# Optimization experiments

Hardware: AMD Instinct MI355X
Metric: run time of the kernel (lower is better)

The kernel has to match this reference:

```python
import jax, jax.numpy as jnp
import numpy as np
from jax import lax

MARGIN = 0.3
BIGF = 1e9


def _pairwise_dist(x):
    # dist[i,j] = ||x_i - x_j||, clamped at 1e-12 before sqrt (as in torch code)
    sq = jnp.sum(x * x, axis=1)
    d = sq[:, None] + sq[None, :] - 2.0 * (x @ x.T)
    return jnp.sqrt(jnp.clip(d, 1e-12))


def _hard_mining(dist, targets):
    is_pos = targets[:, None] == targets[None, :]
    ap = jnp.where(is_pos, dist, jnp.asarray(-BIGF, dist.dtype))
    an = jnp.where(is_pos, jnp.asarray(BIGF, dist.dtype), dist)
    dist_ap = jnp.max(ap, axis=1)
    p_inds = jnp.argmax(ap, axis=1)
    dist_an = jnp.min(an, axis=1)
    n_inds = jnp.argmin(an, axis=1)
    return dist_ap, dist_an, p_inds, n_inds


def _batch_euclidean(x, y):
    # x: [N,m,d], y: [N,n,d] -> [N,m,n]
    xx = jnp.sum(x * x, axis=-1)[:, :, None]
    yy = jnp.sum(y * y, axis=-1)[:, None, :]
    d = xx + yy - 2.0 * jnp.einsum('nmd,nkd->nmk', x, y)
    return jnp.sqrt(jnp.clip(d, 1e-12))


def _shortest_dist(dmat):
    # DTW-style shortest path over [m,n] grid, batched over N: dp[i,j] = d[i,j] + min(dp[i-1,j], dp[i,j-1])
    N, m, n = dmat.shape
    big = jnp.asarray(BIGF, dmat.dtype)
    init_row = jnp.full((N, n), big, dmat.dtype).at[:, 0].set(0.0)  # virtual row -1: only (0,0) reachable

    def row_step(prev_row, drow):  # prev_row,drow: [N,n]
        def col_step(left, un):  # left: [N]
            up, d = un
            cur = d + jnp.minimum(up, left)
            return cur, cur
        _, cols = lax.scan(col_step, jnp.full((N,), big, dmat.dtype), (prev_row.T, drow.T))
        return cols.T, None

    last_row, _ = lax.scan(row_step, init_row, jnp.moveaxis(dmat, 1, 0))
    return last_row[:, -1]


def _batch_local_dist(x, y):
    d = _batch_euclidean(x, y)
    d = jnp.tanh(d * 0.5)  # == (exp(d)-1)/(exp(d)+1), numerically safe
    return _shortest_dist(d)


def _margin_ranking(dist_an, dist_ap, margin):
    # MarginRankingLoss with y=1: mean(relu(margin - (dist_an - dist_ap)))
    return jnp.mean(jnp.maximum(0.0, margin + dist_ap - dist_an))


def setup_inputs() -> dict:
    key = jax.random.key(0)
    k1, k2 = jax.random.split(key)
    N, D = 512, 2048
    LD, PARTS = 128, 8
    K = 4  # instances per identity (PK sampling)
    inputs = jax.random.normal(k1, (N, D), dtype=jnp.float32)
    local_features = jax.random.normal(k2, (N, LD, PARTS), dtype=jnp.float32)
    targets = jnp.arange(N, dtype=jnp.int64) // K
    return {"inputs": inputs, "targets": targets, "local_features": local_features}


def reference(inputs, targets, local_features):
    dist = _pairwise_dist(inputs)
    dist_ap, dist_an, p_inds, n_inds = _hard_mining(dist, targets)
    global_loss = _margin_ranking(dist_an, dist_ap, MARGIN)
    lf = jnp.transpose(local_features, (0, 2, 1))  # [N, parts, local_dim]
    local_ap = _batch_local_dist(lf, lf[p_inds])
    local_an = _batch_local_dist(lf, lf[n_inds])
    local_loss = _margin_ranking(local_an, local_ap, MARGIN)
    return (global_loss, local_loss)
```

## Files before the change

### kernel.cpp

```cpp
#include <hip/hip_runtime.h>
#include <math.h>

#define MARGIN 0.3f
#define BIGF 1e9f
#define NN 512
#define DD 2048
#define LDIM 128
#define PARTS 8

typedef __attribute__((ext_vector_type(8))) __bf16 bf16x8;
typedef __attribute__((ext_vector_type(4))) float f32x4;

__device__ __forceinline__ void cvt8(const float4 a, const float4 b,
                                     bf16x8& h, bf16x8& l) {
    float f[8] = {a.x, a.y, a.z, a.w, b.x, b.y, b.z, b.w};
#pragma unroll
    for (int e = 0; e < 8; e++) {
        __bf16 hh = (__bf16)f[e];
        h[e] = hh;
        l[e] = (__bf16)(f[e] - (float)hh);
    }
}

__global__ __launch_bounds__(256, 2) void k_gram(
    const float* __restrict__ X, float* __restrict__ Gp,
    float* __restrict__ ndiag, float* gsum, float* lsum, unsigned* counter)
{
    __shared__ __bf16 Ah[4096], Al[4096], Bh[4096], Bl[4096];

    int bid = blockIdx.x;
    int tj = bid & 7, ti = (bid >> 3) & 7, ks = bid >> 6;
    int t = threadIdx.x;
    int w = t >> 6, lane = t & 63;
    int wr = w >> 1, wc = w & 1;

    if (bid == 0 && t == 0) { *gsum = 0.0f; *lsum = 0.0f; *counter = 0u; }

    int m = t >> 7;
    int r = (t >> 1) & 63;
    int kst = t & 1;
    int grow = (m ? tj : ti) * 64 + r;
    const float4* gp4 = (const float4*)(X + (size_t)grow * DD + ks * 256 + kst * 32);
    int ebase = kst * 2048 + (r >> 4) * 512 + (r & 15) * 8;
    __bf16* hb = (m ? Bh : Ah) + ebase;
    __bf16* lb = (m ? Bl : Al) + ebase;

    float4 cur[8];
#pragma unroll
    for (int q = 0; q < 8; q++) cur[q] = gp4[q];

    f32x4 acc00 = {0.f, 0.f, 0.f, 0.f};
    f32x4 acc01 = {0.f, 0.f, 0.f, 0.f};
    f32x4 acc10 = {0.f, 0.f, 0.f, 0.f};
    f32x4 acc11 = {0.f, 0.f, 0.f, 0.f};

#pragma unroll
    for (int it = 0; it < 4; ++it) {
        if (it > 0) __syncthreads();
#pragma unroll
        for (int jg = 0; jg < 4; jg++) {
            bf16x8 h, l;
            cvt8(cur[2 * jg], cur[2 * jg + 1], h, l);
            *(bf16x8*)(hb + jg * 128) = h;
            *(bf16x8*)(lb + jg * 128) = l;
        }
        if (it < 3) {
            const float4* np = gp4 + (it + 1) * 16;
#pragma unroll
            for (int q = 0; q < 8; q++) cur[q] = np[q];
        }
        __syncthreads();

#pragma unroll
        for (int kstep = 0; kstep < 2; kstep++) {
            const bf16x8* fAh = (const bf16x8*)&Ah[kstep * 2048 + wr * 1024];
            const bf16x8* fAl = (const bf16x8*)&Al[kstep * 2048 + wr * 1024];
            const bf16x8* fBh = (const bf16x8*)&Bh[kstep * 2048 + wc * 1024];
            const bf16x8* fBl = (const bf16x8*)&Bl[kstep * 2048 + wc * 1024];
            bf16x8 ah0 = fAh[lane], ah1 = fAh[lane + 64];
            bf16x8 al0 = fAl[lane], al1 = fAl[lane + 64];
            bf16x8 bh0 = fBh[lane], bh1 = fBh[lane + 64];
            bf16x8 bl0 = fBl[lane], bl1 = fBl[lane + 64];

            acc00 = __builtin_amdgcn_mfma_f32_16x16x32_bf16(ah0, bh0, acc00, 0, 0, 0);
            acc00 = __builtin_amdgcn_mfma_f32_16x16x32_bf16(ah0, bl0, acc00, 0, 0, 0);
            acc00 = __builtin_amdgcn_mfma_f32_16x16x32_bf16(al0, bh0, acc00, 0, 0, 0);

            acc01 = __builtin_amdgcn_mfma_f32_16x16x32_bf16(ah0, bh1, acc01, 0, 0, 0);
            acc01 = __builtin_amdgcn_mfma_f32_16x16x32_bf16(ah0, bl1, acc01, 0, 0, 0);
            acc01 = __builtin_amdgcn_mfma_f32_16x16x32_bf16(al0, bh1, acc01, 0, 0, 0);

            acc10 = __builtin_amdgcn_mfma_f32_16x16x32_bf16(ah1, bh0, acc10, 0, 0, 0);
            acc10 = __builtin_amdgcn_mfma_f32_16x16x32_bf16(ah1, bl0, acc10, 0, 0, 0);
            acc10 = __builtin_amdgcn_mfma_f32_16x16x32_bf16(al1, bh0, acc10, 0, 0, 0);

            acc11 = __builtin_amdgcn_mfma_f32_16x16x32_bf16(ah1, bh1, acc11, 0, 0, 0);
            acc11 = __builtin_amdgcn_mfma_f32_16x16x32_bf16(ah1, bl1, acc11, 0, 0, 0);
            acc11 = __builtin_amdgcn_mfma_f32_16x16x32_bf16(al1, bh1, acc11, 0, 0, 0);
        }
    }

    int rbase = ti * 64 + wr * 32 + ((lane >> 4) << 2);
    int cbase = tj * 64 + wc * 32 + (lane & 15);
    float* gb = Gp + (size_t)ks * NN * NN;
    f32x4 accs[2][2] = {{acc00, acc01}, {acc10, acc11}};
#pragma unroll
    for (int g = 0; g < 2; g++)
#pragma unroll
        for (int h = 0; h < 2; h++)
#pragma unroll
            for (int rr = 0; rr < 4; rr++)
                gb[(size_t)(rbase + g * 16 + rr) * NN + cbase + h * 16] = accs[g][h][rr];

    if (ti == tj && wr == wc && ((lane >> 4) == ((lane & 15) >> 2))) {
        int rr = lane & 3;
        int row0 = rbase + rr;
        ndiag[ks * NN + row0]      = acc00[rr];
        ndiag[ks * NN + row0 + 16] = acc11[rr];
    }
}

__global__ __launch_bounds__(256) void k_mine_local(
    const float* __restrict__ Gp, const float* __restrict__ ndiag,
    const int* __restrict__ tg, const float* __restrict__ LF,
    float* gsum, float* lsum, unsigned* counter, float* __restrict__ out)
{
    __shared__ float sdiag[NN];
    __shared__ float s_apv[4]; __shared__ int s_api[4];
    __shared__ float s_anv[4]; __shared__ int s_ani[4];
    __shared__ int sh_pn[2];
    __shared__ float A[LDIM * PARTS];
    __shared__ float B[2][LDIM * PARTS];
    __shared__ float dtm[2][64];
    __shared__ float res[2];

    int i = blockIdx.x;
    int t = threadIdx.x;

    float d0 = 0.f, d1 = 0.f;
#pragma unroll
    for (int ks = 0; ks < 8; ks++) {
        d0 += ndiag[ks * NN + t];
        d1 += ndiag[ks * NN + t + 256];
    }
    sdiag[t] = d0;
    sdiag[t + 256] = d1;
    __syncthreads();

    float ni = sdiag[i];
    int tgt_i = tg[i];

    float apv = -BIGF; int api = 0x7fffffff;
    float anv =  BIGF; int ani = 0x7fffffff;

#pragma unroll
    for (int jj = 0; jj < 2; jj++) {
        int j = t + jj * 256;
        float g = 0.f;
#pragma unroll
        for (int ks = 0; ks < 8; ks++)
            g += Gp[(size_t)ks * NN * NN + (size_t)i * NN + j];
        float nj = (jj == 0) ? d0 : d1;
        float dd = ni + nj - 2.0f * g;
        float dist = sqrtf(fmaxf(dd, 1e-12f));
        bool pos = (tg[j] == tgt_i);
        float a = pos ? dist : -BIGF;
        if (a > apv || (a == apv && j < api)) { apv = a; api = j; }
        float b = pos ? BIGF : dist;
        if (b < anv || (b == anv && j < ani)) { anv = b; ani = j; }
    }
    for (int off = 32; off > 0; off >>= 1) {
        float av = __shfl_down(apv, off); int ai = __shfl_down(api, off);
        if (av > apv || (av == apv && ai < api)) { apv = av; api = ai; }
        float nv = __shfl_down(anv, off); int nid = __shfl_down(ani, off);
        if (nv < anv || (nv == anv && nid < ani)) { anv = nv; ani = nid; }
    }
    int lane = t & 63, wid = t >> 6;
    if (lane == 0) { s_apv[wid] = apv; s_api[wid] = api;
                     s_anv[wid] = anv; s_ani[wid] = ani; }
    __syncthreads();
    if (t == 0) {
        apv = s_apv[0]; api = s_api[0]; anv = s_anv[0]; ani = s_ani[0];
        for (int wv = 1; wv < 4; wv++) {
            float av = s_apv[wv]; int ai = s_api[wv];
            if (av > apv || (av == apv && ai < api)) { apv = av; api = ai; }
            float nv = s_anv[wv]; int nid = s_ani[wv];
            if (nv < anv || (nv == anv && nid < ani)) { anv = nv; ani = nid; }
        }
        sh_pn[0] = api;
        sh_pn[1] = ani;
        atomicAdd(gsum, fmaxf(0.0f, MARGIN + apv - anv));
    }
    __syncthreads();

    int w = t >> 6;
    ((float4*)A)[t] = ((const float4*)(LF + (size_t)i * LDIM * PARTS))[t];
    if (w < 2) {
        int ind = sh_pn[w];
        const float4* B4 = (const float4*)(LF + (size_t)ind * LDIM * PARTS);
        float4* Bw = (float4*)B[w];
        Bw[lane]       = B4[lane];
        Bw[lane + 64]  = B4[lane + 64];
        Bw[lane + 128] = B4[lane + 128];
        Bw[lane + 192] = B4[lane + 192];
    }
    __syncthreads();

    if (w < 2) {
        int p = lane >> 3, q = lane & 7;
        float acc = 0.0f;
        const float* Bw = B[w];
        for (int d = 0; d < LDIM; d++) {
            float diff = A[d * PARTS + p] - Bw[d * PARTS + q];
            acc = fmaf(diff, diff, acc);
        }
        float dist = sqrtf(fmaxf(acc, 1e-12f));
        dtm[w][p * 8 + q] = tanhf(0.5f * dist);
    }
    __syncthreads();

    if ((t == 0) || (t == 64)) {
        const float* dm = dtm[w];
        float dp[8];
        dp[0] = dm[0];
        for (int j = 1; j < 8; j++) dp[j] = dp[j - 1] + dm[j];
        for (int rr = 1; rr < 8; rr++) {
            dp[0] += dm[rr * 8];
            for (int j = 1; j < 8; j++)
                dp[j] = dm[rr * 8 + j] + fminf(dp[j], dp[j - 1]);
        }
        res[w] = dp[7];
    }
    __syncthreads();

    if (t == 0) {
        float l = fmaxf(0.0f, MARGIN + res[0] - res[1]);
        atomicAdd(lsum, l);
        __threadfence();
        unsigned old = atomicAdd(counter, 1u);
        if (old == (NN - 1)) {
            __threadfence();
            float ls = atomicAdd(lsum, 0.0f);
            float gs = atomicAdd(gsum, 0.0f);
            out[0] = gs * (1.0f / NN);
            out[1] = ls * (1.0f / NN);
        }
    }
}

extern "C" void kernel_launch(void* const* d_in, const int* in_sizes, int n_in,
                              void* d_out, int out_size, void* d_ws, size_t ws_size,
                              hipStream_t stream)
{
    const float* X  = (const float*)d_in[0];
    const int*   tg = (const int*)d_in[1];
    const float* LF = (const float*)d_in[2];
    float* out = (float*)d_out;

    char* ws = (char*)d_ws;
    float*    Gp      = (float*)ws;
    float*    ndiag   = (float*)(ws + (8u << 20));
    float*    gsum    = (float*)(ws + (8u << 20) + 16384);
    float*    lsum    = (float*)(ws + (8u << 20) + 16388);
    unsigned* counter = (unsigned*)(ws + (8u << 20) + 16392);

    k_gram<<<512, 256, 0, stream>>>(X, Gp, ndiag, gsum, lsum, counter);
    k_mine_local<<<512, 256, 0, stream>>>(Gp, ndiag, tg, LF, gsum, lsum, counter, out);
}
```

Measured before the change: 96.93 us.

## Fuse gram and mining kernels with a software grid barrier

Merges the split-K gram kernel and the hard-mining/local-distance kernel into one launch, separated by a global atomic spin barrier over all 512 blocks. Counters are now zeroed with a memset on the stream instead of inside the kernel. This removes the second kernel launch and the gap between launches, but it adds a memset, a grid-wide spin wait, and more shared memory per block. The barrier depends on all 512 blocks being resident at once, which the 2-blocks-per-SM launch bound is meant to allow.

Result: slower. 195.4 us (+101.6%).

```diff
diff --git a/kernel.cpp b/kernel.cpp
--- a/kernel.cpp
+++ b/kernel.cpp
@@ -22,19 +22,27 @@
     }
 }
 
-__global__ __launch_bounds__(256, 2) void k_gram(
-    const float* __restrict__ X, float* __restrict__ Gp,
-    float* __restrict__ ndiag, float* gsum, float* lsum, unsigned* counter)
+__global__ __launch_bounds__(256, 2) void k_fused(
+    const float* __restrict__ X, const int* __restrict__ tg,
+    const float* __restrict__ LF, float* __restrict__ Gp,
+    float* __restrict__ ndiag, float* gsum, float* lsum,
+    unsigned* ticket, unsigned* bar, float* __restrict__ out)
 {
     __shared__ __bf16 Ah[4096], Al[4096], Bh[4096], Bl[4096];
+    __shared__ float sdiag[NN];
+    __shared__ float s_apv[4]; __shared__ int s_api[4];
+    __shared__ float s_anv[4]; __shared__ int s_ani[4];
+    __shared__ int sh_pn[2];
+    __shared__ float A2[LDIM * PARTS];
+    __shared__ float B2[2][LDIM * PARTS];
+    __shared__ float dtm[2][64];
+    __shared__ float res[2];
 
     int bid = blockIdx.x;
     int tj = bid & 7, ti = (bid >> 3) & 7, ks = bid >> 6;
     int t = threadIdx.x;
     int w = t >> 6, lane = t & 63;
     int wr = w >> 1, wc = w & 1;
-
-    if (bid == 0 && t == 0) { *gsum = 0.0f; *lsum = 0.0f; *counter = 0u; }
 
     int m = t >> 7;
     int r = (t >> 1) & 63;
@@ -118,30 +126,25 @@
         ndiag[ks * NN + row0]      = acc00[rr];
         ndiag[ks * NN + row0 + 16] = acc11[rr];
     }
-}
-
-__global__ __launch_bounds__(256) void k_mine_local(
-    const float* __restrict__ Gp, const float* __restrict__ ndiag,
-    const int* __restrict__ tg, const float* __restrict__ LF,
-    float* gsum, float* lsum, unsigned* counter, float* __restrict__ out)
-{
-    __shared__ float sdiag[NN];
-    __shared__ float s_apv[4]; __shared__ int s_api[4];
-    __shared__ float s_anv[4]; __shared__ int s_ani[4];
-    __shared__ int sh_pn[2];
-    __shared__ float A[LDIM * PARTS];
-    __shared__ float B[2][LDIM * PARTS];
-    __shared__ float dtm[2][64];
-    __shared__ float res[2];
-
-    int i = blockIdx.x;
-    int t = threadIdx.x;
+
+    __syncthreads();
+    if (t == 0) {
+        __threadfence();
+        __hip_atomic_fetch_add(bar, 1u, __ATOMIC_RELEASE, __HIP_MEMORY_SCOPE_AGENT);
+        while (__hip_atomic_load(bar, __ATOMIC_ACQUIRE, __HIP_MEMORY_SCOPE_AGENT)
+               < (unsigned)NN)
+            __builtin_amdgcn_s_sleep(2);
+    }
+    __syncthreads();
+    __threadfence();
+
+    int i = bid;
 
     float d0 = 0.f, d1 = 0.f;
 #pragma unroll
-    for (int ks = 0; ks < 8; ks++) {
-        d0 += ndiag[ks * NN + t];
-        d1 += ndiag[ks * NN + t + 256];
+    for (int kk = 0; kk < 8; kk++) {
+        d0 += ndiag[kk * NN + t];
+        d1 += ndiag[kk * NN + t + 256];
     }
     sdiag[t] = d0;
     sdiag[t + 256] = d1;
@@ -158,8 +161,8 @@
         int j = t + jj * 256;
         float g = 0.f;
 #pragma unroll
-        for (int ks = 0; ks < 8; ks++)
-            g += Gp[(size_t)ks * NN * NN + (size_t)i * NN + j];
+        for (int kk = 0; kk < 8; kk++)
+            g += Gp[(size_t)kk * NN * NN + (size_t)i * NN + j];
         float nj = (jj == 0) ? d0 : d1;
         float dd = ni + nj - 2.0f * g;
         float dist = sqrtf(fmaxf(dd, 1e-12f));
@@ -175,9 +178,8 @@
         float nv = __shfl_down(anv, off); int nid = __shfl_down(ani, off);
         if (nv < anv || (nv == anv && nid < ani)) { anv = nv; ani = nid; }
     }
-    int lane = t & 63, wid = t >> 6;
-    if (lane == 0) { s_apv[wid] = apv; s_api[wid] = api;
-                     s_anv[wid] = anv; s_ani[wid] = ani; }
+    if (lane == 0) { s_apv[w] = apv; s_api[w] = api;
+                     s_anv[w] = anv; s_ani[w] = ani; }
     __syncthreads();
     if (t == 0) {
         apv = s_apv[0]; api = s_api[0]; anv = s_anv[0]; ani = s_ani[0];
@@ -193,12 +195,11 @@
     }
     __syncthreads();
 
-    int w = t >> 6;
-    ((float4*)A)[t] = ((const float4*)(LF + (size_t)i * LDIM * PARTS))[t];
+    ((float4*)A2)[t] = ((const float4*)(LF + (size_t)i * LDIM * PARTS))[t];
     if (w < 2) {
         int ind = sh_pn[w];
         const float4* B4 = (const float4*)(LF + (size_t)ind * LDIM * PARTS);
-        float4* Bw = (float4*)B[w];
+        float4* Bw = (float4*)B2[w];
         Bw[lane]       = B4[lane];
         Bw[lane + 64]  = B4[lane + 64];
         Bw[lane + 128] = B4[lane + 128];
@@ -209,9 +210,9 @@
     if (w < 2) {
         int p = lane >> 3, q = lane & 7;
         float acc = 0.0f;
-        const float* Bw = B[w];
+        const float* Bw = B2[w];
         for (int d = 0; d < LDIM; d++) {
-            float diff = A[d * PARTS + p] - Bw[d * PARTS + q];
+            float diff = A2[d * PARTS + p] - Bw[d * PARTS + q];
             acc = fmaf(diff, diff, acc);
         }
         float dist = sqrtf(fmaxf(acc, 1e-12f));
@@ -237,7 +238,7 @@
         float l = fmaxf(0.0f, MARGIN + res[0] - res[1]);
         atomicAdd(lsum, l);
         __threadfence();
-        unsigned old = atomicAdd(counter, 1u);
+        unsigned old = atomicAdd(ticket, 1u);
         if (old == (NN - 1)) {
             __threadfence();
             float ls = atomicAdd(lsum, 0.0f);
@@ -260,10 +261,13 @@
     char* ws = (char*)d_ws;
     float*    Gp      = (float*)ws;
     float*    ndiag   = (float*)(ws + (8u << 20));
-    float*    gsum    = (float*)(ws + (8u << 20) + 16384);
-    float*    lsum    = (float*)(ws + (8u << 20) + 16388);
-    unsigned* counter = (unsigned*)(ws + (8u << 20) + 16392);
-
-    k_gram<<<512, 256, 0, stream>>>(X, Gp, ndiag, gsum, lsum, counter);
-    k_mine_local<<<512, 256, 0, stream>>>(Gp, ndiag, tg, LF, gsum, lsum, counter, out);
+    char*     ctr     = ws + (8u << 20) + 16384;
+    float*    gsum    = (float*)(ctr + 0);
+    float*    lsum    = (float*)(ctr + 4);
+    unsigned* ticket  = (unsigned*)(ctr + 8);
+    unsigned* bar     = (unsigned*)(ctr + 12);
+
+    hipMemsetAsync(ctr, 0, 16, stream);
+    k_fused<<<NN, 256, 0, stream>>>(X, tg, LF, Gp, ndiag, gsum, lsum,
+                                    ticket, bar, out);
 }
```

## Drop bf16 split-precision correction terms and double-buffer LDS tiles in gram kernel

Applied to the files above, without the earlier changes.

The Gram-matrix kernel no longer splits each fp32 value into high and low bf16 parts. It now issues one bf16 MFMA per tile pair instead of three, which cuts MFMA work and LDS traffic by about two thirds. The shared tiles are also double-buffered, so the next chunk is converted and written during the current compute and one barrier per iteration is removed. The cost is that pairwise distances now carry only bf16 precision. That can change the hard-mining argmax/argmin picks and the loss values relative to the fp32 reference.

Result: faster. 94.97 us (-2.0%).

```diff
diff --git a/kernel.cpp b/kernel.cpp
--- a/kernel.cpp
+++ b/kernel.cpp
@@ -11,22 +11,11 @@
 typedef __attribute__((ext_vector_type(8))) __bf16 bf16x8;
 typedef __attribute__((ext_vector_type(4))) float f32x4;
 
-__device__ __forceinline__ void cvt8(const float4 a, const float4 b,
-                                     bf16x8& h, bf16x8& l) {
-    float f[8] = {a.x, a.y, a.z, a.w, b.x, b.y, b.z, b.w};
-#pragma unroll
-    for (int e = 0; e < 8; e++) {
-        __bf16 hh = (__bf16)f[e];
-        h[e] = hh;
-        l[e] = (__bf16)(f[e] - (float)hh);
-    }
-}
-
 __global__ __launch_bounds__(256, 2) void k_gram(
     const float* __restrict__ X, float* __restrict__ Gp,
     float* __restrict__ ndiag, float* gsum, float* lsum, unsigned* counter)
 {
-    __shared__ __bf16 Ah[4096], Al[4096], Bh[4096], Bl[4096];
+    __shared__ __bf16 A[2][4096], B[2][4096];
 
     int bid = blockIdx.x;
     int tj = bid & 7, ti = (bid >> 3) & 7, ks = bid >> 6;
@@ -42,8 +31,6 @@
     int grow = (m ? tj : ti) * 64 + r;
     const float4* gp4 = (const float4*)(X + (size_t)grow * DD + ks * 256 + kst * 32);
     int ebase = kst * 2048 + (r >> 4) * 512 + (r & 15) * 8;
-    __bf16* hb = (m ? Bh : Ah) + ebase;
-    __bf16* lb = (m ? Bl : Al) + ebase;
 
     float4 cur[8];
 #pragma unroll
@@ -54,49 +41,51 @@
     f32x4 acc10 = {0.f, 0.f, 0.f, 0.f};
     f32x4 acc11 = {0.f, 0.f, 0.f, 0.f};
 
+    {
+        __bf16* hb = (m ? B[0] : A[0]) + ebase;
+#pragma unroll
+        for (int jg = 0; jg < 4; jg++) {
+            float fe[8] = {cur[2 * jg].x, cur[2 * jg].y, cur[2 * jg].z, cur[2 * jg].w,
+                           cur[2 * jg + 1].x, cur[2 * jg + 1].y, cur[2 * jg + 1].z, cur[2 * jg + 1].w};
+            bf16x8 h;
+#pragma unroll
+            for (int e = 0; e < 8; e++) h[e] = (__bf16)fe[e];
+            *(bf16x8*)(hb + jg * 128) = h;
+        }
+    }
+
 #pragma unroll
     for (int it = 0; it < 4; ++it) {
-        if (it > 0) __syncthreads();
-#pragma unroll
-        for (int jg = 0; jg < 4; jg++) {
-            bf16x8 h, l;
-            cvt8(cur[2 * jg], cur[2 * jg + 1], h, l);
-            *(bf16x8*)(hb + jg * 128) = h;
-            *(bf16x8*)(lb + jg * 128) = l;
-        }
+        __syncthreads();
         if (it < 3) {
             const float4* np = gp4 + (it + 1) * 16;
 #pragma unroll
             for (int q = 0; q < 8; q++) cur[q] = np[q];
         }
-        __syncthreads();
-
+        int buf = it & 1;
 #pragma unroll
         for (int kstep = 0; kstep < 2; kstep++) {
-            const bf16x8* fAh = (const bf16x8*)&Ah[kstep * 2048 + wr * 1024];
-            const bf16x8* fAl = (const bf16x8*)&Al[kstep * 2048 + wr * 1024];
-            const bf16x8* fBh = (const bf16x8*)&Bh[kstep * 2048 + wc * 1024];
-            const bf16x8* fBl = (const bf16x8*)&Bl[kstep * 2048 + wc * 1024];
-            bf16x8 ah0 = fAh[lane], ah1 = fAh[lane + 64];
-            bf16x8 al0 = fAl[lane], al1 = fAl[lane + 64];
-            bf16x8 bh0 = fBh[lane], bh1 = fBh[lane + 64];
-            bf16x8 bl0 = fBl[lane], bl1 = fBl[lane + 64];
-
+            const bf16x8* fA = (const bf16x8*)&A[buf][kstep * 2048 + wr * 1024];
+            const bf16x8* fB = (const bf16x8*)&B[buf][kstep * 2048 + wc * 1024];
+            bf16x8 ah0 = fA[lane], ah1 = fA[lane + 64];
+            bf16x8 bh0 = fB[lane], bh1 = fB[lane + 64];
             acc00 = __builtin_amdgcn_mfma_f32_16x16x32_bf16(ah0, bh0, acc00, 0, 0, 0);
-            acc00 = __builtin_amdgcn_mfma_f32_16x16x32_bf16(ah0, bl0, acc00, 0, 0, 0);
-            acc00 = __builtin_amdgcn_mfma_f32_16x16x32_bf16(al0, bh0, acc00, 0, 0, 0);
-
             acc01 = __builtin_amdgcn_mfma_f32_16x16x32_bf16(ah0, bh1, acc01, 0, 0, 0);
-            acc01 = __builtin_amdgcn_mfma_f32_16x16x32_bf16(ah0, bl1, acc01, 0, 0, 0);
-            acc01 = __builtin_amdgcn_mfma_f32_16x16x32_bf16(al0, bh1, acc01, 0, 0, 0);
-
             acc10 = __builtin_amdgcn_mfma_f32_16x16x32_bf16(ah1, bh0, acc10, 0, 0, 0);
-            acc10 = __builtin_amdgcn_mfma_f32_16x16x32_bf16(ah1, bl0, acc10, 0, 0, 0);
-            acc10 = __builtin_amdgcn_mfma_f32_16x16x32_bf16(al1, bh0, acc10, 0, 0, 0);
-
             acc11 = __builtin_amdgcn_mfma_f32_16x16x32_bf16(ah1, bh1, acc11, 0, 0, 0);
-            acc11 = __builtin_amdgcn_mfma_f32_16x16x32_bf16(ah1, bl1, acc11, 0, 0, 0);
-            acc11 = __builtin_amdgcn_mfma_f32_16x16x32_bf16(al1, bh1, acc11, 0, 0, 0);
+        }
+        if (it < 3) {
+            int nb = (it + 1) & 1;
+            __bf16* hb = (m ? B[nb] : A[nb]) + ebase;
+#pragma unroll
+            for (int jg = 0; jg < 4; jg++) {
+                float fe[8] = {cur[2 * jg].x, cur[2 * jg].y, cur[2 * jg].z, cur[2 * jg].w,
+                               cur[2 * jg + 1].x, cur[2 * jg + 1].y, cur[2 * jg + 1].z, cur[2 * jg + 1].w};
+                bf16x8 h;
+#pragma unroll
+                for (int e = 0; e < 8; e++) h[e] = (__bf16)fe[e];
+                *(bf16x8*)(hb + jg * 128) = h;
+            }
         }
     }
 
@@ -129,8 +118,8 @@
     __shared__ float s_apv[4]; __shared__ int s_api[4];
     __shared__ float s_anv[4]; __shared__ int s_ani[4];
     __shared__ int sh_pn[2];
-    __shared__ float A[LDIM * PARTS];
-    __shared__ float B[2][LDIM * PARTS];
+    __shared__ float A2[LDIM * PARTS];
+    __shared__ float B2[2][LDIM * PARTS];
     __shared__ float dtm[2][64];
     __shared__ float res[2];
 
@@ -194,11 +183,11 @@
     __syncthreads();
 
     int w = t >> 6;
-    ((float4*)A)[t] = ((const float4*)(LF + (size_t)i * LDIM * PARTS))[t];
+    ((float4*)A2)[t] = ((const float4*)(LF + (size_t)i * LDIM * PARTS))[t];
     if (w < 2) {
         int ind = sh_pn[w];
         const float4* B4 = (const float4*)(LF + (size_t)ind * LDIM * PARTS);
-        float4* Bw = (float4*)B[w];
+        float4* Bw = (float4*)B2[w];
         Bw[lane]       = B4[lane];
         Bw[lane + 64]  = B4[lane + 64];
         Bw[lane + 128] = B4[lane + 128];
@@ -209,9 +198,9 @@
     if (w < 2) {
         int p = lane >> 3, q = lane & 7;
         float acc = 0.0f;
-        const float* Bw = B[w];
+        const float* Bw = B2[w];
         for (int d = 0; d < LDIM; d++) {
-            float diff = A[d * PARTS + p] - Bw[d * PARTS + q];
+            float diff = A2[d * PARTS + p] - Bw[d * PARTS + q];
             acc = fmaf(diff, diff, acc);
         }
         float dist = sqrtf(fmaxf(acc, 1e-12f));
```
